# Kernel optimization log

Measured on AMD Instinct MI355X. Metric: run time of the kernel, lower is better.

Reference implementation:

```python
import jax, jax.numpy as jnp
import numpy as np

B, N, P, K, D = 8, 2048, 64, 32, 384
DEPTH, DI, DS, DCONV, DTR, NC = 12, 768, 16, 4, 24, 40
BN_EPS = 1e-5


def _spread_bits(v):
    v = v & 1023
    v = (v | (v << 16)) & 50331903
    v = (v | (v << 8)) & 50393103
    v = (v | (v << 4)) & 51130563
    v = (v | (v << 2)) & 153391689
    return v


def _zkey(x, y, z):
    return _spread_bits(x) | (_spread_bits(y) << 1) | (_spread_bits(z) << 2)


def _sfc_order(xyz, trans):
    lo = xyz.min(0, keepdims=True)
    hi = xyz.max(0, keepdims=True)
    q = jnp.clip(((xyz - lo) / (hi - lo + 1e-6) * 1023.0).astype(jnp.int32), 0, 1023)
    if trans:
        keys = _zkey(q[:, 2], q[:, 1], q[:, 0])
    else:
        keys = _zkey(q[:, 0], q[:, 1], q[:, 2])
    return jnp.argsort(keys)


def _ln(x, g, b):
    m = x.mean(-1, keepdims=True)
    v = jnp.var(x, axis=-1, keepdims=True)
    return (x - m) / jnp.sqrt(v + 1e-5) * g + b


def _bn_eval(x, g, b):
    # BatchNorm in eval mode, running_mean=0 / running_var=1
    return x * (g / np.float32(np.sqrt(1.0 + BN_EPS))) + b


def _patch_embed_one(xyz, w1, b1, g1, be1, w2, b2, g2, be2, w3, b3, g3, be3):
    # xyz: (N,3)
    cidx = (jnp.arange(P) * (N / P)).astype(jnp.int32)
    centers = xyz[cidx]                                      # (P,3)
    d2 = ((centers[:, None, :] - xyz[None, :, :]) ** 2).sum(-1)  # (P,N)
    _, knn = jax.lax.top_k(-d2, K)                           # (P,K) smallest dists
    nx = xyz[knn] - centers[:, None, :]                      # (P,K,3)
    h = jax.nn.gelu(_bn_eval(nx @ w1.T + b1, g1, be1), approximate=False)   # (P,K,64)
    h = jax.nn.gelu(_bn_eval(h @ w2.T + b2, g2, be2), approximate=False)    # (P,K,128)
    h = _bn_eval(h @ w3.T + b3, g3, be3)                     # (P,K,384)
    return h.max(1), centers


def _mamba(x, in_w, conv_w, conv_b, xp_w, dt_w, dt_b, Alog, Dp, out_w):
    # x: (B,L,D)
    Bsz, L, _ = x.shape
    xz = x @ in_w.T                                          # (B,L,2*DI)
    xc, z = xz[..., :DI], xz[..., DI:]
    xpad = jnp.pad(xc, ((0, 0), (DCONV - 1, 0), (0, 0)))
    xc = sum(xpad[:, j:j + L, :] * conv_w[:, j] for j in range(DCONV)) + conv_b
    xc = jax.nn.silu(xc)
    x_dbl = xc @ xp_w.T                                      # (B,L,DTR+2*DS)
    dt = x_dbl[..., :DTR]
    Bm = x_dbl[..., DTR:DTR + DS]
    Cm = x_dbl[..., DTR + DS:]
    delta = jax.nn.softplus(dt @ dt_w.T + dt_b)              # (B,L,DI)
    A = -jnp.exp(Alog)                                       # (DI,DS)

    def step(h, inp):
        d_t, B_t, C_t, u_t = inp                             # (B,DI),(B,DS),(B,DS),(B,DI)
        h = h * jnp.exp(d_t[..., None] * A) + (d_t * u_t)[..., None] * B_t[:, None, :]
        return h, jnp.einsum('bds,bs->bd', h, C_t)

    h0 = jnp.zeros((Bsz, DI, DS), x.dtype)
    inps = (delta.transpose(1, 0, 2), Bm.transpose(1, 0, 2),
            Cm.transpose(1, 0, 2), xc.transpose(1, 0, 2))
    _, ys = jax.lax.scan(step, h0, inps)                     # (L,B,DI)
    y = ys.transpose(1, 0, 2) + Dp * xc
    y = y * jax.nn.silu(z)
    return y @ out_w.T


def setup_inputs() -> dict:
    key = jax.random.key(0)
    ks = iter(jax.random.split(key, 64))
    nrm = lambda *s: jax.random.normal(next(ks), s, jnp.float32) * 0.02
    inp = {
        'data': jax.random.normal(next(ks), (B, N, 3), jnp.float32),
        'pe_w1': nrm(64, 3), 'pe_b1': jnp.zeros(64), 'pe_g1': jnp.ones(64), 'pe_be1': jnp.zeros(64),
        'pe_w2': nrm(128, 64), 'pe_b2': jnp.zeros(128), 'pe_g2': jnp.ones(128), 'pe_be2': jnp.zeros(128),
        'pe_w3': nrm(D, 128), 'pe_b3': jnp.zeros(D), 'pe_g3': jnp.ones(D), 'pe_be3': jnp.zeros(D),
        'oi_h_scale': jnp.ones(D), 'oi_h_shift': jnp.zeros(D),
        'oi_th_scale': jnp.ones(D), 'oi_th_shift': jnp.zeros(D),
        'pos_embed': nrm(1, P, D),
        'blk_ln_g': jnp.ones((DEPTH, D)), 'blk_ln_b': jnp.zeros((DEPTH, D)),
        'blk_in_w': nrm(DEPTH, 2 * DI, D),
        'blk_conv_w': nrm(DEPTH, DI, DCONV), 'blk_conv_b': jnp.zeros((DEPTH, DI)),
        'blk_xp_w': nrm(DEPTH, DTR + 2 * DS, DI),
        'blk_dt_w': nrm(DEPTH, DI, DTR), 'blk_dt_b': jnp.full((DEPTH, DI), -4.0),
        'blk_Alog': jnp.tile(jnp.log(jnp.arange(1, DS + 1, dtype=jnp.float32)), (DEPTH, DI, 1)),
        'blk_D': jnp.ones((DEPTH, DI)),
        'blk_out_w': nrm(DEPTH, D, DI),
        'norm_g': jnp.ones(D), 'norm_b': jnp.zeros(D),
        'mlp_w1': nrm(256, D), 'mlp_b1': jnp.zeros(256),
        'mlp_w2': nrm(64, 256), 'mlp_b2': jnp.zeros(64),
        'mlp_w3': nrm(NC, 64), 'mlp_b3': jnp.zeros(NC),
    }
    return inp


def reference(data, pe_w1, pe_b1, pe_g1, pe_be1, pe_w2, pe_b2, pe_g2, pe_be2,
              pe_w3, pe_b3, pe_g3, pe_be3, oi_h_scale, oi_h_shift, oi_th_scale,
              oi_th_shift, pos_embed, blk_ln_g, blk_ln_b, blk_in_w, blk_conv_w,
              blk_conv_b, blk_xp_w, blk_dt_w, blk_dt_b, blk_Alog, blk_D,
              blk_out_w, norm_g, norm_b, mlp_w1, mlp_b1, mlp_w2, mlp_b2,
              mlp_w3, mlp_b3):
    xyz = data[:, :, :3]
    tokens, centers = jax.vmap(
        _patch_embed_one, in_axes=(0,) + (None,) * 12)(
        xyz, pe_w1, pe_b1, pe_g1, pe_be1, pe_w2, pe_b2, pe_g2, pe_be2,
        pe_w3, pe_b3, pe_g3, pe_be3)                         # (B,P,D),(B,P,3)
    order_h = jax.vmap(lambda c: _sfc_order(c, False))(centers)
    order_th = jax.vmap(lambda c: _sfc_order(c, True))(centers)
    th = jnp.take_along_axis(tokens, order_h[:, :, None], axis=1) * oi_h_scale + oi_h_shift
    tth = jnp.take_along_axis(tokens, order_th[:, :, None], axis=1) * oi_th_scale + oi_th_shift
    t = jnp.concatenate([th + pos_embed, tth + pos_embed], axis=1)  # (B,2P,D)
    for i in range(DEPTH):
        t = t + _mamba(_ln(t, blk_ln_g[i], blk_ln_b[i]),
                       blk_in_w[i], blk_conv_w[i], blk_conv_b[i], blk_xp_w[i],
                       blk_dt_w[i], blk_dt_b[i], blk_Alog[i], blk_D[i], blk_out_w[i])
    t = _ln(t, norm_g, norm_b)
    x = t.mean(1)
    x = jax.nn.relu(x @ mlp_w1.T + mlp_b1)
    x = jax.nn.relu(x @ mlp_w2.T + mlp_b2)
    return x @ mlp_w3.T + mlp_b3
```

## Files before the change

### kernel.cpp

```cpp
#include <hip/hip_runtime.h>
#include <math.h>

#define BB 8
#define NN 2048
#define PP 64
#define KK 32
#define DD 384
#define DEPTH 12
#define DI 768
#define DS 16
#define DCONV 4
#define DTR 24
#define NC 40
#define LL 128
#define XROW (DTR + 2 * DS)
#define NR (BB * LL)

using bf16x8 = __attribute__((ext_vector_type(8))) short;
using floatx4 = __attribute__((ext_vector_type(4))) float;

__device__ __forceinline__ float gelu_exact(float x) {
    return 0.5f * x * (1.0f + erff(x * 0.70710678118654752440f));
}
__device__ __forceinline__ float siluf(float x) {
    return x / (1.0f + expf(-x));
}
__device__ __forceinline__ unsigned short f2bf(float f) {
    unsigned u = __float_as_uint(f);
    u += 0x7fffu + ((u >> 16) & 1u);
    return (unsigned short)(u >> 16);
}
__device__ __forceinline__ float bf2f(short s) {
    return __uint_as_float(((unsigned)(unsigned short)s) << 16);
}
__device__ __forceinline__ unsigned spread_bits(unsigned v) {
    v &= 1023u;
    v = (v | (v << 16)) & 50331903u;
    v = (v | (v << 8)) & 50393103u;
    v = (v | (v << 4)) & 51130563u;
    v = (v | (v << 2)) & 153391689u;
    return v;
}

__global__ void k_cvt(const float* __restrict__ in_w, const float* __restrict__ out_w,
                      const float* __restrict__ pe_w3, const float* __restrict__ xp,
                      unsigned short* __restrict__ inwbf, unsigned short* __restrict__ owbf,
                      unsigned short* __restrict__ w3bf, unsigned short* __restrict__ xpbf)
{
    int idx = (blockIdx.x * 256 + threadIdx.x) * 4;
    const int n1 = DEPTH * 2 * DI * DD;
    const int n2 = DEPTH * DD * DI;
    const int n3 = DD * 128;
    const int n4 = DEPTH * 64 * DI;
    if (idx < n1) {
        float4 v = *(const float4*)(in_w + idx);
        ushort4 o; o.x = f2bf(v.x); o.y = f2bf(v.y); o.z = f2bf(v.z); o.w = f2bf(v.w);
        *(ushort4*)(inwbf + idx) = o;
        return;
    }
    idx -= n1;
    if (idx < n2) {
        float4 v = *(const float4*)(out_w + idx);
        ushort4 o; o.x = f2bf(v.x); o.y = f2bf(v.y); o.z = f2bf(v.z); o.w = f2bf(v.w);
        *(ushort4*)(owbf + idx) = o;
        return;
    }
    idx -= n2;
    if (idx < n3) {
        float4 v = *(const float4*)(pe_w3 + idx);
        ushort4 o; o.x = f2bf(v.x); o.y = f2bf(v.y); o.z = f2bf(v.z); o.w = f2bf(v.w);
        *(ushort4*)(w3bf + idx) = o;
        return;
    }
    idx -= n3;
    if (idx < n4) {
        int i = idx / (64 * DI);
        int rem = idx - i * 64 * DI;
        int n = rem / DI, k = rem % DI;
        ushort4 o;
        if (n < XROW) {
            float4 v = *(const float4*)(xp + (size_t)i * XROW * DI + (size_t)n * DI + k);
            o.x = f2bf(v.x); o.y = f2bf(v.y); o.z = f2bf(v.z); o.w = f2bf(v.w);
        } else {
            o.x = o.y = o.z = o.w = 0;
        }
        *(ushort4*)(xpbf + (size_t)i * 64 * DI + (size_t)n * DI + k) = o;
    }
}

__global__ __launch_bounds__(256) void k_patch(
    const float* __restrict__ data,
    const float* __restrict__ w1, const float* __restrict__ b1,
    const float* __restrict__ g1, const float* __restrict__ be1,
    const float* __restrict__ w2, const float* __restrict__ b2,
    const float* __restrict__ g2, const float* __restrict__ be2,
    const unsigned short* __restrict__ w3bf, const float* __restrict__ b3,
    const float* __restrict__ g3, const float* __restrict__ be3,
    float* __restrict__ tokens, float* __restrict__ centers)
{
    const int bp = blockIdx.x;
    const int b = bp >> 6, p = bp & 63;
    const int tid = threadIdx.x;
    const float* X = data + (size_t)b * NN * 3;
    const float inv_den = 0.99999500003749968752f;

    __shared__ unsigned long long wred[4];
    __shared__ int klist[KK];
    __shared__ float nxs[KK * 3];
    __shared__ float h1s[KK * 64];
    __shared__ short h2b[KK * 136];

    const float cx = X[p * 32 * 3 + 0];
    const float cy = X[p * 32 * 3 + 1];
    const float cz = X[p * 32 * 3 + 2];
    if (tid == 0) {
        centers[(b * PP + p) * 3 + 0] = cx;
        centers[(b * PP + p) * 3 + 1] = cy;
        centers[(b * PP + p) * 3 + 2] = cz;
    }

    {
        const int lane = tid & 63, wid = tid >> 6;
        unsigned long long pk[8];
#pragma unroll
        for (int q = 0; q < 8; q++) {
            int i = tid + 256 * q;
            float dx = cx - X[i * 3 + 0];
            float dy = cy - X[i * 3 + 1];
            float dz = cz - X[i * 3 + 2];
            float d2 = dx * dx + dy * dy + dz * dz;
            pk[q] = ((unsigned long long)__float_as_uint(d2) << 32) | (unsigned)i;
        }
        for (int k = 0; k < KK; k++) {
            unsigned long long m = pk[0];
#pragma unroll
            for (int q = 1; q < 8; q++) m = pk[q] < m ? pk[q] : m;
#pragma unroll
            for (int off = 32; off; off >>= 1) {
                unsigned long long o = __shfl_xor(m, off);
                m = o < m ? o : m;
            }
            if (lane == 0) wred[wid] = m;
            __syncthreads();
            unsigned long long g = wred[0];
#pragma unroll
            for (int w = 1; w < 4; w++) g = wred[w] < g ? wred[w] : g;
#pragma unroll
            for (int q = 0; q < 8; q++)
                if (pk[q] == g) pk[q] = ~0ull;
            if (tid == 0) klist[k] = (int)(g & 0xffffffffu);
            __syncthreads();
        }
    }

    if (tid < KK) {
        int q = klist[tid];
        nxs[tid * 3 + 0] = X[q * 3 + 0] - cx;
        nxs[tid * 3 + 1] = X[q * 3 + 1] - cy;
        nxs[tid * 3 + 2] = X[q * 3 + 2] - cz;
    }
    __syncthreads();

    for (int e = tid; e < KK * 64; e += 256) {
        int j = e >> 6, c = e & 63;
        float v = nxs[j * 3 + 0] * w1[c * 3 + 0] + nxs[j * 3 + 1] * w1[c * 3 + 1] +
                  nxs[j * 3 + 2] * w1[c * 3 + 2] + b1[c];
        v = v * (g1[c] * inv_den) + be1[c];
        h1s[j * 64 + c] = gelu_exact(v);
    }
    __syncthreads();

    for (int e = tid; e < KK * 128; e += 256) {
        int j = e >> 7, c = e & 127;
        const float4* wr = (const float4*)(w2 + (size_t)c * 64);
        const float4* hr = (const float4*)(h1s + j * 64);
        float acc = 0.f;
#pragma unroll
        for (int q = 0; q < 16; q++) {
            float4 wv = wr[q], hv = hr[q];
            acc += hv.x * wv.x + hv.y * wv.y + hv.z * wv.z + hv.w * wv.w;
        }
        float v = (acc + b2[c]) * (g2[c] * inv_den) + be2[c];
        h2b[j * 136 + c] = (short)f2bf(gelu_exact(v));
    }
    __syncthreads();

    const int wave = tid >> 6, lane = tid & 63;
    const int quad = lane >> 4, r = lane & 15;
    floatx4 acc3[2][6] = {};
#pragma unroll
    for (int ks = 0; ks < 4; ks++) {
        const int k0 = ks * 32;
        bf16x8 af[2];
        af[0] = *(const bf16x8*)(h2b + (size_t)r * 136 + quad * 8 + k0);
        af[1] = *(const bf16x8*)(h2b + (size_t)(16 + r) * 136 + quad * 8 + k0);
        bf16x8 bfv[6];
#pragma unroll
        for (int nj = 0; nj < 6; nj++) {
            int n = wave * 96 + nj * 16 + r;
            bfv[nj] = *(const bf16x8*)(w3bf + (size_t)n * 128 + quad * 8 + k0);
        }
#pragma unroll
        for (int mi = 0; mi < 2; mi++)
#pragma unroll
            for (int nj = 0; nj < 6; nj++)
                acc3[mi][nj] = __builtin_amdgcn_mfma_f32_16x16x32_bf16(af[mi], bfv[nj], acc3[mi][nj], 0, 0, 0);
    }
#pragma unroll
    for (int nj = 0; nj < 6; nj++) {
        int col = wave * 96 + nj * 16 + r;
        float sc = g3[col] * inv_den;
        float offc = b3[col] * sc + be3[col];
        float m = -3.4e38f;
#pragma unroll
        for (int mi = 0; mi < 2; mi++)
#pragma unroll
            for (int r2 = 0; r2 < 4; r2++)
                m = fmaxf(m, acc3[mi][nj][r2] * sc + offc);
        m = fmaxf(m, __shfl_xor(m, 16));
        m = fmaxf(m, __shfl_xor(m, 32));
        if (quad == 0) tokens[(size_t)bp * DD + col] = m;
    }
}

__global__ __launch_bounds__(256) void k_sfc_build(
    const float* __restrict__ centers, const float* __restrict__ tokens,
    const float* __restrict__ hs, const float* __restrict__ hb,
    const float* __restrict__ ts2, const float* __restrict__ tb2,
    const float* __restrict__ pos, float* __restrict__ tout)
{
    const int b = blockIdx.y, part = blockIdx.x;
    const int tid = threadIdx.x;

    __shared__ float csh[PP][3];
    __shared__ float slo[3], shi[3];
    __shared__ unsigned khs[PP], kts[PP];
    __shared__ int oh[PP], ot[PP];

    if (tid < PP) {
        csh[tid][0] = centers[(b * PP + tid) * 3 + 0];
        csh[tid][1] = centers[(b * PP + tid) * 3 + 1];
        csh[tid][2] = centers[(b * PP + tid) * 3 + 2];
    }
    __syncthreads();
    if (tid == 0) {
        for (int k = 0; k < 3; k++) {
            float lo = csh[0][k], hi = csh[0][k];
            for (int j = 1; j < PP; j++) { lo = fminf(lo, csh[j][k]); hi = fmaxf(hi, csh[j][k]); }
            slo[k] = lo; shi[k] = hi;
        }
    }
    __syncthreads();
    if (tid < PP) {
        int q[3];
        for (int k = 0; k < 3; k++) {
            float t = (csh[tid][k] - slo[k]) / (shi[k] - slo[k] + 1e-6f) * 1023.0f;
            int qi = (int)t;
            qi = qi < 0 ? 0 : (qi > 1023 ? 1023 : qi);
            q[k] = qi;
        }
        khs[tid] = spread_bits((unsigned)q[0]) | (spread_bits((unsigned)q[1]) << 1) |
                   (spread_bits((unsigned)q[2]) << 2);
        kts[tid] = spread_bits((unsigned)q[2]) | (spread_bits((unsigned)q[1]) << 1) |
                   (spread_bits((unsigned)q[0]) << 2);
    }
    __syncthreads();
    if (tid < PP) {
        unsigned kh = khs[tid], kt = kts[tid];
        int rh = 0, rt = 0;
        for (int j = 0; j < PP; j++) {
            unsigned a = khs[j];
            rh += (a < kh) || (a == kh && j < tid);
            unsigned c = kts[j];
            rt += (c < kt) || (c == kt && j < tid);
        }
        oh[rh] = tid;
        ot[rt] = tid;
    }
    __syncthreads();

    const int base = part * (LL * DD / 24);
    for (int e = tid; e < LL * DD / 24; e += 256) {
        int idx = base + e;
        int d = idx % DD;
        int l = idx / DD;
        float v;
        if (l < PP) {
            int src = oh[l];
            v = tokens[((size_t)b * PP + src) * DD + d] * hs[d] + hb[d] + pos[l * DD + d];
        } else {
            int l2 = l - PP;
            int src = ot[l2];
            v = tokens[((size_t)b * PP + src) * DD + d] * ts2[d] + tb2[d] + pos[l2 * DD + d];
        }
        tout[(size_t)b * LL * DD + idx] = v;
    }
}

__global__ __launch_bounds__(256) void k_stats(const float* __restrict__ t,
                                               const float* __restrict__ g,
                                               const float* __restrict__ gb,
                                               unsigned short* __restrict__ tbf,
                                               float* __restrict__ xdbl)
{
    const int tid = threadIdx.x;
    {
        int gi = blockIdx.x * 256 + tid;
        if (gi < NR * XROW) xdbl[gi] = 0.f;
    }
    const int wid = tid >> 6, lane = tid & 63;
    const int row = blockIdx.x * 4 + wid;
    const size_t base = (size_t)row * DD;
    float v[6];
    float s = 0.f, q = 0.f;
#pragma unroll
    for (int j = 0; j < 6; j++) {
        v[j] = t[base + lane + 64 * j];
        s += v[j]; q += v[j] * v[j];
    }
#pragma unroll
    for (int off = 32; off; off >>= 1) { s += __shfl_xor(s, off); q += __shfl_xor(q, off); }
    float mean = s * (1.0f / DD);
    float var = q * (1.0f / DD) - mean * mean;
    float inv = 1.0f / sqrtf(var + 1e-5f);
#pragma unroll
    for (int j = 0; j < 6; j++) {
        int i = lane + 64 * j;
        tbf[base + i] = f2bf((v[j] - mean) * inv * g[i] + gb[i]);
    }
}

__global__ __launch_bounds__(256) void k_mfma_xz(
    const unsigned short* __restrict__ tbf,
    const unsigned short* __restrict__ inwbf,
    const float* __restrict__ cw, const float* __restrict__ cb,
    const unsigned short* __restrict__ xpbf,
    unsigned short* __restrict__ xcbf, unsigned short* __restrict__ zsbf,
    float* __restrict__ xdbl)
{
    __shared__ short ct[128][72];
    const int tid = threadIdx.x;
    const int wave = tid >> 6, lane = tid & 63;
    const int quad = lane >> 4, r = lane & 15;
    const int wm = wave >> 1, wn = wave & 1;
    const int b = blockIdx.y;
    const int n0 = blockIdx.x * 64;
    const int m0 = b * 128 + wm * 64;

    floatx4 acc[4][2] = {};
    const unsigned short* Ab = tbf + (size_t)(m0 + r) * DD + quad * 8;
    const unsigned short* Bb = inwbf + (size_t)(n0 + wn * 32 + r) * DD + quad * 8;
    for (int k0 = 0; k0 < DD; k0 += 32) {
        bf16x8 af[4], bfv[2];
#pragma unroll
        for (int i = 0; i < 4; i++)
            af[i] = *(const bf16x8*)(Ab + (size_t)(i * 16) * DD + k0);
#pragma unroll
        for (int j = 0; j < 2; j++)
            bfv[j] = *(const bf16x8*)(Bb + (size_t)(j * 16) * DD + k0);
#pragma unroll
        for (int i = 0; i < 4; i++)
#pragma unroll
            for (int j = 0; j < 2; j++)
                acc[i][j] = __builtin_amdgcn_mfma_f32_16x16x32_bf16(af[i], bfv[j], acc[i][j], 0, 0, 0);
    }

#pragma unroll
    for (int i = 0; i < 4; i++)
#pragma unroll
        for (int r2 = 0; r2 < 4; r2++) {
            short* cp = &ct[wm * 64 + i * 16 + quad * 4 + r2][wn * 32 + r];
#pragma unroll
            for (int j = 0; j < 2; j++)
                cp[j * 16] = (short)f2bf(acc[i][j][r2]);
        }
    __syncthreads();

    const int l0 = (tid >> 3) * 4;
    const int c0 = (tid & 7) * 8;
    if (n0 < DI) {
        float cwv[8][4], cbv[8];
#pragma unroll
        for (int q = 0; q < 8; q++) {
            *(float4*)cwv[q] = *(const float4*)(cw + (size_t)(n0 + c0 + q) * 4);
            cbv[q] = cb[n0 + c0 + q];
        }
        unsigned short ov[4][8];
#pragma unroll
        for (int dl = 0; dl < 4; dl++) {
            const int l = l0 + dl;
            float u[8];
#pragma unroll
            for (int q = 0; q < 8; q++) u[q] = cbv[q];
#pragma unroll
            for (int j = 0; j < DCONV; j++) {
                int lt = l - (DCONV - 1) + j;
                if (lt >= 0) {
                    bf16x8 x = *(const bf16x8*)&ct[lt][c0];
#pragma unroll
                    for (int q = 0; q < 8; q++) u[q] += bf2f(x[q]) * cwv[q][j];
                }
            }
#pragma unroll
            for (int q = 0; q < 8; q++) ov[dl][q] = f2bf(siluf(u[q]));
        }
        __syncthreads();
#pragma unroll
        for (int dl = 0; dl < 4; dl++) {
            const int l = l0 + dl;
            *(bf16x8*)&ct[l][c0] = *(bf16x8*)ov[dl];
            *(bf16x8*)(xcbf + (size_t)(b * LL + l) * DI + n0 + c0) = *(bf16x8*)ov[dl];
        }
        __syncthreads();

        floatx4 acc2[2][4] = {};
#pragma unroll
        for (int k0 = 0; k0 < 64; k0 += 32) {
            bf16x8 af2[2], bfv2[4];
#pragma unroll
            for (int i = 0; i < 2; i++)
                af2[i] = *(const bf16x8*)&ct[wave * 32 + i * 16 + r][k0 + quad * 8];
#pragma unroll
            for (int nj = 0; nj < 4; nj++)
                bfv2[nj] = *(const bf16x8*)(xpbf + (size_t)(nj * 16 + r) * DI + n0 + k0 + quad * 8);
#pragma unroll
            for (int i = 0; i < 2; i++)
#pragma unroll
                for (int nj = 0; nj < 4; nj++)
                    acc2[i][nj] = __builtin_amdgcn_mfma_f32_16x16x32_bf16(af2[i], bfv2[nj], acc2[i][nj], 0, 0, 0);
        }
#pragma unroll
        for (int i = 0; i < 2; i++)
#pragma unroll
            for (int nj = 0; nj < 4; nj++) {
                int col = nj * 16 + r;
                if (col < XROW) {
#pragma unroll
                    for (int r2 = 0; r2 < 4; r2++) {
                        int row = b * LL + wave * 32 + i * 16 + quad * 4 + r2;
                        unsafeAtomicAdd(&xdbl[(size_t)row * XROW + col], acc2[i][nj][r2]);
                    }
                }
            }
    } else {
        const int nz = n0 - DI;
#pragma unroll
        for (int dl = 0; dl < 4; dl++) {
            const int l = l0 + dl;
            bf16x8 x = *(const bf16x8*)&ct[l][c0];
            unsigned short o[8];
#pragma unroll
            for (int q = 0; q < 8; q++) o[q] = f2bf(siluf(bf2f(x[q])));
            *(bf16x8*)(zsbf + (size_t)(b * LL + l) * DI + nz + c0) = *(bf16x8*)o;
        }
    }
}

__global__ __launch_bounds__(128) void k_scan(
    const float* __restrict__ xdbl,
    const unsigned short* __restrict__ xcbf, const unsigned short* __restrict__ zsbf,
    const float* __restrict__ dtw, const float* __restrict__ dtb,
    const float* __restrict__ Alog, const float* __restrict__ Dp,
    unsigned short* __restrict__ ybf)
{
    const int tid = threadIdx.x;
    const int b = blockIdx.x / DI;
    const int d = blockIdx.x % DI;

    __shared__ float sdel[LL];
    __shared__ float sdus[LL];
    __shared__ float sus[LL];
    __shared__ float szs[LL];
    __shared__ float negA[DS];
    __shared__ float ApL[DS][9];
    __shared__ float HlL[DS][9];
    __shared__ float hst[DS][9];

    {
        const int t = tid;
        const size_t row = (size_t)b * LL + t;
        const float* xd = xdbl + row * XROW;
        const float* w = dtw + d * DTR;
        float acc = dtb[d];
#pragma unroll
        for (int k = 0; k < DTR; k += 4) {
            float4 xv = *(const float4*)(xd + k);
            float4 wv = *(const float4*)(w + k);
            acc += xv.x * wv.x + xv.y * wv.y + xv.z * wv.z + xv.w * wv.w;
        }
        float delta = fmaxf(acc, 0.f) + log1pf(__expf(-fabsf(acc)));
        float u = bf2f((short)xcbf[row * DI + d]);
        sdel[t] = delta;
        sdus[t] = delta * u;
        sus[t] = u;
        szs[t] = bf2f((short)zsbf[row * DI + d]);
    }
    if (tid < DS) negA[tid] = -__expf(Alog[d * DS + tid]);
    __syncthreads();

    const int s = tid & 15;
    const int c = tid >> 4;
    const float* xB = xdbl + ((size_t)b * LL + c * 16) * XROW + DTR + s;

    float a_r[16], duB_r[16], C_r[16];
    {
        float h = 0.f, Ap = 1.f;
        const float na = negA[s];
#pragma unroll
        for (int q = 0; q < 16; q++) {
            int t = c * 16 + q;
            float a = __expf(sdel[t] * na);
            float Bv = xB[(size_t)q * XROW];
            float Cv = xB[(size_t)q * XROW + DS];
            a_r[q] = a;
            duB_r[q] = sdus[t] * Bv;
            C_r[q] = Cv;
            h = h * a + duB_r[q];
            Ap *= a;
        }
        ApL[s][c] = Ap;
        HlL[s][c] = h;
    }
    __syncthreads();
    if (tid < DS) {
        float hs = 0.f;
#pragma unroll
        for (int cc = 0; cc < 8; cc++) {
            hst[tid][cc] = hs;
            hs = ApL[tid][cc] * hs + HlL[tid][cc];
        }
    }
    __syncthreads();

    {
        const float Dd = Dp[d];
        float h = hst[s][c];
        unsigned short* yc = ybf + ((size_t)b * LL + c * 16) * DI + d;
#pragma unroll
        for (int q = 0; q < 16; q++) {
            h = h * a_r[q] + duB_r[q];
            float p = h * C_r[q];
            p += __shfl_xor(p, 1, 16);
            p += __shfl_xor(p, 2, 16);
            p += __shfl_xor(p, 4, 16);
            p += __shfl_xor(p, 8, 16);
            if (s == 0) {
                int t = c * 16 + q;
                yc[(size_t)q * DI] = f2bf((p + Dd * sus[t]) * szs[t]);
            }
        }
    }
}

__global__ __launch_bounds__(256) void k_mfma_op(
    const unsigned short* __restrict__ ybf,
    const unsigned short* __restrict__ owbf,
    float* __restrict__ t)
{
    const int tid = threadIdx.x;
    const int wave = tid >> 6, lane = tid & 63;
    const int quad = lane >> 4, r = lane & 15;
    const int wr2 = wave >> 1, wc = wave & 1;
    const int n0 = blockIdx.x * 64 + wc * 32;
    const int m0 = blockIdx.y * 32 + wr2 * 16;

    floatx4 acc[2] = {};
    const unsigned short* Ab = ybf + (size_t)(m0 + r) * DI + quad * 8;
    const unsigned short* Bb = owbf + (size_t)(n0 + r) * DI + quad * 8;
    for (int k0 = 0; k0 < DI; k0 += 32) {
        bf16x8 af = *(const bf16x8*)(Ab + k0);
        bf16x8 b0 = *(const bf16x8*)(Bb + k0);
        bf16x8 b1 = *(const bf16x8*)(Bb + (size_t)16 * DI + k0);
        acc[0] = __builtin_amdgcn_mfma_f32_16x16x32_bf16(af, b0, acc[0], 0, 0, 0);
        acc[1] = __builtin_amdgcn_mfma_f32_16x16x32_bf16(af, b1, acc[1], 0, 0, 0);
    }

#pragma unroll
    for (int j = 0; j < 2; j++) {
        int col = n0 + j * 16 + r;
#pragma unroll
        for (int r2 = 0; r2 < 4; r2++) {
            int row = m0 + quad * 4 + r2;
            float* tp = t + (size_t)row * DD + col;
            *tp += acc[j][r2];
        }
    }
}

__global__ __launch_bounds__(256) void k_lnpool(const float* __restrict__ t,
                                                const float* __restrict__ ng,
                                                const float* __restrict__ nb,
                                                float* __restrict__ pparts)
{
    const int b = blockIdx.y, chunk = blockIdx.x;
    const int tid = threadIdx.x;
    const int wave = tid >> 6, lane = tid & 63;
    __shared__ float pw[4][DD];

    for (int c = lane; c < DD; c += 64) pw[wave][c] = 0.f;
    __syncthreads();

    for (int rr = 0; rr < 4; rr++) {
        const int row = b * LL + chunk * 16 + wave * 4 + rr;
        const float* xr = t + (size_t)row * DD;
        float v[6];
        float s = 0.f, q = 0.f;
#pragma unroll
        for (int j = 0; j < 6; j++) { v[j] = xr[lane + 64 * j]; s += v[j]; q += v[j] * v[j]; }
#pragma unroll
        for (int off = 32; off; off >>= 1) { s += __shfl_xor(s, off); q += __shfl_xor(q, off); }
        float mean = s * (1.0f / DD);
        float var = q * (1.0f / DD) - mean * mean;
        float inv = 1.0f / sqrtf(var + 1e-5f);
#pragma unroll
        for (int j = 0; j < 6; j++) {
            int c = lane + 64 * j;
            pw[wave][c] += (v[j] - mean) * inv * ng[c] + nb[c];
        }
    }
    __syncthreads();
    float* out = pparts + ((size_t)b * 8 + chunk) * DD;
    for (int c = tid; c < DD; c += 256)
        out[c] = pw[0][c] + pw[1][c] + pw[2][c] + pw[3][c];
}

__global__ __launch_bounds__(256) void k_mlp(const float* __restrict__ pparts,
    const float* __restrict__ w1, const float* __restrict__ b1,
    const float* __restrict__ w2, const float* __restrict__ b2,
    const float* __restrict__ w3, const float* __restrict__ b3,
    float* __restrict__ out)
{
    const int b = blockIdx.x, tid = threadIdx.x;
    __shared__ float pl[DD];
    __shared__ float h1[256];
    __shared__ float h2[64];
    for (int c = tid; c < DD; c += 256) {
        const float* pp = pparts + (size_t)b * 8 * DD + c;
        float s = 0.f;
#pragma unroll
        for (int z = 0; z < 8; z++) s += pp[z * DD];
        pl[c] = s * (1.0f / LL);
    }
    __syncthreads();

    {
        float acc = b1[tid];
        const float* wr = w1 + (size_t)tid * DD;
        for (int k = 0; k < DD; k++) acc += pl[k] * wr[k];
        h1[tid] = fmaxf(acc, 0.f);
    }
    __syncthreads();
    if (tid < 64) {
        float acc = b2[tid];
        const float* wr = w2 + (size_t)tid * 256;
        for (int k = 0; k < 256; k++) acc += h1[k] * wr[k];
        h2[tid] = fmaxf(acc, 0.f);
    }
    __syncthreads();
    if (tid < NC) {
        float acc = b3[tid];
        const float* wr = w3 + (size_t)tid * 64;
        for (int k = 0; k < 64; k++) acc += h2[k] * wr[k];
        out[b * NC + tid] = acc;
    }
}

extern "C" void kernel_launch(void* const* d_in, const int* in_sizes, int n_in,
                              void* d_out, int out_size, void* d_ws, size_t ws_size,
                              hipStream_t stream)
{
    const float* data      = (const float*)d_in[0];
    const float* pe_w1     = (const float*)d_in[1];
    const float* pe_b1     = (const float*)d_in[2];
    const float* pe_g1     = (const float*)d_in[3];
    const float* pe_be1    = (const float*)d_in[4];
    const float* pe_w2     = (const float*)d_in[5];
    const float* pe_b2     = (const float*)d_in[6];
    const float* pe_g2     = (const float*)d_in[7];
    const float* pe_be2    = (const float*)d_in[8];
    const float* pe_w3     = (const float*)d_in[9];
    const float* pe_b3     = (const float*)d_in[10];
    const float* pe_g3     = (const float*)d_in[11];
    const float* pe_be3    = (const float*)d_in[12];
    const float* oi_h_scale  = (const float*)d_in[13];
    const float* oi_h_shift  = (const float*)d_in[14];
    const float* oi_th_scale = (const float*)d_in[15];
    const float* oi_th_shift = (const float*)d_in[16];
    const float* pos_embed = (const float*)d_in[17];
    const float* blk_ln_g  = (const float*)d_in[18];
    const float* blk_ln_b  = (const float*)d_in[19];
    const float* blk_in_w  = (const float*)d_in[20];
    const float* blk_conv_w = (const float*)d_in[21];
    const float* blk_conv_b = (const float*)d_in[22];
    const float* blk_xp_w  = (const float*)d_in[23];
    const float* blk_dt_w  = (const float*)d_in[24];
    const float* blk_dt_b  = (const float*)d_in[25];
    const float* blk_Alog  = (const float*)d_in[26];
    const float* blk_D     = (const float*)d_in[27];
    const float* blk_out_w = (const float*)d_in[28];
    const float* norm_g    = (const float*)d_in[29];
    const float* norm_b    = (const float*)d_in[30];
    const float* mlp_w1    = (const float*)d_in[31];
    const float* mlp_b1    = (const float*)d_in[32];
    const float* mlp_w2    = (const float*)d_in[33];
    const float* mlp_b2    = (const float*)d_in[34];
    const float* mlp_w3    = (const float*)d_in[35];
    const float* mlp_b3    = (const float*)d_in[36];

    float* ws = (float*)d_ws;
    size_t off = 0;
    auto alloc = [&](size_t n) { float* p = ws + off; off += (n + 63) & ~(size_t)63; return p; };
    float* tokens  = alloc((size_t)BB * PP * DD);
    float* centers = alloc((size_t)BB * PP * 3);
    float* t    = alloc((size_t)NR * DD);
    float* xdbl = alloc((size_t)NR * XROW);
    float* pparts  = alloc((size_t)BB * 8 * DD);
    unsigned short* tbf   = (unsigned short*)alloc((size_t)NR * DD / 2);
    unsigned short* xcbf  = (unsigned short*)alloc((size_t)NR * DI / 2);
    unsigned short* zsbf  = (unsigned short*)alloc((size_t)NR * DI / 2);
    unsigned short* ybf   = (unsigned short*)alloc((size_t)NR * DI / 2);
    unsigned short* inwbf = (unsigned short*)alloc((size_t)DEPTH * 2 * DI * DD / 2);
    unsigned short* owbf  = (unsigned short*)alloc((size_t)DEPTH * DD * DI / 2);
    unsigned short* xpbf  = (unsigned short*)alloc((size_t)DEPTH * 64 * DI / 2);
    unsigned short* w3bf  = (unsigned short*)alloc((size_t)DD * 128 / 2);

    {
        const int total = DEPTH * 2 * DI * DD + DEPTH * DD * DI + DD * 128 + DEPTH * 64 * DI;
        k_cvt<<<(total / 4 + 255) / 256, 256, 0, stream>>>(
            blk_in_w, blk_out_w, pe_w3, blk_xp_w, inwbf, owbf, w3bf, xpbf);
    }

    k_patch<<<BB * PP, 256, 0, stream>>>(data,
        pe_w1, pe_b1, pe_g1, pe_be1, pe_w2, pe_b2, pe_g2, pe_be2,
        w3bf, pe_b3, pe_g3, pe_be3, tokens, centers);
    k_sfc_build<<<dim3(24, BB), 256, 0, stream>>>(centers, tokens,
        oi_h_scale, oi_h_shift, oi_th_scale, oi_th_shift, pos_embed, t);

    for (int i = 0; i < DEPTH; i++) {
        const float* ln_g = blk_ln_g + i * DD;
        const float* ln_b = blk_ln_b + i * DD;
        const float* cw   = blk_conv_w + (size_t)i * DI * DCONV;
        const float* cb   = blk_conv_b + (size_t)i * DI;
        const float* dtw  = blk_dt_w + (size_t)i * DI * DTR;
        const float* dtb  = blk_dt_b + (size_t)i * DI;
        const float* Al   = blk_Alog + (size_t)i * DI * DS;
        const float* Dpp  = blk_D + (size_t)i * DI;
        const unsigned short* inw = inwbf + (size_t)i * 2 * DI * DD;
        const unsigned short* ow  = owbf + (size_t)i * DD * DI;
        const unsigned short* xpb = xpbf + (size_t)i * 64 * DI;

        k_stats<<<NR / 4, 256, 0, stream>>>(t, ln_g, ln_b, tbf, xdbl);
        k_mfma_xz<<<dim3(24, BB), 256, 0, stream>>>(
            tbf, inw, cw, cb, xpb, xcbf, zsbf, xdbl);
        k_scan<<<BB * DI, 128, 0, stream>>>(xdbl, xcbf, zsbf, dtw, dtb, Al, Dpp, ybf);
        k_mfma_op<<<dim3(DD / 64, NR / 32), 256, 0, stream>>>(ybf, ow, t);
    }

    k_lnpool<<<dim3(8, BB), 256, 0, stream>>>(t, norm_g, norm_b, pparts);
    k_mlp<<<BB, 256, 0, stream>>>(pparts, mlp_w1, mlp_b1, mlp_w2, mlp_b2, mlp_w3, mlp_b3,
                                  (float*)d_out);
}
```

Before: 960.6 us.

## Replace iterative kNN argmin with radix select and split-K out-projection

The kNN selection in the patch kernel swaps 32 rounds of block-wide argmin reductions for a 4-pass byte-wise radix select over distance keys. Keys below the threshold are collected with atomics, and ties are broken by index on a single thread. Separately, the out-projection GEMM is split over K into two halves that accumulate into the residual with float atomics, which doubles the block count. The atomic accumulation makes float summation order nondeterministic, and neighbour order in klist changes, though the max-pool downstream does not depend on it.

Measured after the change: 937.9 us. -2.4%, faster.

```diff
diff --git a/kernel.cpp b/kernel.cpp
--- a/kernel.cpp
+++ b/kernel.cpp
@@ -104,8 +104,10 @@
     const float* X = data + (size_t)b * NN * 3;
     const float inv_den = 0.99999500003749968752f;
 
-    __shared__ unsigned long long wred[4];
+    __shared__ int hist[256];
     __shared__ int klist[KK];
+    __shared__ int eqlist[256];
+    __shared__ int s_kth, s_byte, s_cnt, s_eqcnt;
     __shared__ float nxs[KK * 3];
     __shared__ float h1s[KK * 64];
     __shared__ short h2b[KK * 136];
@@ -117,11 +119,12 @@
         centers[(b * PP + p) * 3 + 0] = cx;
         centers[(b * PP + p) * 3 + 1] = cy;
         centers[(b * PP + p) * 3 + 2] = cz;
+        s_kth = KK; s_cnt = 0; s_eqcnt = 0;
     }
 
     {
         const int lane = tid & 63, wid = tid >> 6;
-        unsigned long long pk[8];
+        unsigned key[8];
 #pragma unroll
         for (int q = 0; q < 8; q++) {
             int i = tid + 256 * q;
@@ -129,28 +132,71 @@
             float dy = cy - X[i * 3 + 1];
             float dz = cz - X[i * 3 + 2];
             float d2 = dx * dx + dy * dy + dz * dz;
-            pk[q] = ((unsigned long long)__float_as_uint(d2) << 32) | (unsigned)i;
-        }
-        for (int k = 0; k < KK; k++) {
-            unsigned long long m = pk[0];
-#pragma unroll
-            for (int q = 1; q < 8; q++) m = pk[q] < m ? pk[q] : m;
-#pragma unroll
-            for (int off = 32; off; off >>= 1) {
-                unsigned long long o = __shfl_xor(m, off);
-                m = o < m ? o : m;
+            key[q] = __float_as_uint(d2);
+        }
+        unsigned prefix = 0;
+        for (int rnd = 3; rnd >= 0; rnd--) {
+            const int sh = rnd * 8;
+            const unsigned pmask = (rnd == 3) ? 0u : (0xFFFFFFFFu << (8 * (rnd + 1)));
+            hist[tid] = 0;
+            __syncthreads();
+#pragma unroll
+            for (int q = 0; q < 8; q++)
+                if ((key[q] & pmask) == prefix)
+                    atomicAdd(&hist[(key[q] >> sh) & 255], 1);
+            __syncthreads();
+            if (wid == 0) {
+                int c[4], tot = 0;
+#pragma unroll
+                for (int j = 0; j < 4; j++) { c[j] = hist[lane * 4 + j]; tot += c[j]; }
+                int inc = tot;
+#pragma unroll
+                for (int off = 1; off < 64; off <<= 1) {
+                    int u = __shfl_up(inc, off);
+                    if (lane >= off) inc += u;
+                }
+                int exc = inc - tot;
+                int kth = s_kth;
+                bool has = (exc < kth) && (exc + tot >= kth);
+                unsigned long long bal = __ballot(has);
+                int src = __ffsll(bal) - 1;
+                if (lane == src) {
+                    int rem = kth - exc;
+                    int j = 0, cum = 0;
+                    while (cum + c[j] < rem) { cum += c[j]; j++; }
+                    s_byte = lane * 4 + j;
+                    s_kth = rem - cum;
+                }
             }
-            if (lane == 0) wred[wid] = m;
             __syncthreads();
-            unsigned long long g = wred[0];
-#pragma unroll
-            for (int w = 1; w < 4; w++) g = wred[w] < g ? wred[w] : g;
-#pragma unroll
-            for (int q = 0; q < 8; q++)
-                if (pk[q] == g) pk[q] = ~0ull;
-            if (tid == 0) klist[k] = (int)(g & 0xffffffffu);
-            __syncthreads();
-        }
+            prefix |= ((unsigned)s_byte) << sh;
+        }
+        const unsigned kstar = prefix;
+        const int need = s_kth;
+#pragma unroll
+        for (int q = 0; q < 8; q++) {
+            int i = tid + 256 * q;
+            if (key[q] < kstar) {
+                int pos = atomicAdd(&s_cnt, 1);
+                klist[pos] = i;
+            } else if (key[q] == kstar) {
+                int pos = atomicAdd(&s_eqcnt, 1);
+                if (pos < 256) eqlist[pos] = i;
+            }
+        }
+        __syncthreads();
+        if (tid == 0) {
+            int base = s_cnt;
+            int ne = s_eqcnt < 256 ? s_eqcnt : 256;
+            for (int k = 0; k < need; k++) {
+                int best = 0x7fffffff, bi = 0;
+                for (int j = 0; j < ne; j++)
+                    if (eqlist[j] < best) { best = eqlist[j]; bi = j; }
+                klist[base + k] = best;
+                eqlist[bi] = 0x7fffffff;
+            }
+        }
+        __syncthreads();
     }
 
     if (tid < KK) {
@@ -563,11 +609,12 @@
     const int wr2 = wave >> 1, wc = wave & 1;
     const int n0 = blockIdx.x * 64 + wc * 32;
     const int m0 = blockIdx.y * 32 + wr2 * 16;
+    const int kb = blockIdx.z * (DI / 2);
 
     floatx4 acc[2] = {};
-    const unsigned short* Ab = ybf + (size_t)(m0 + r) * DI + quad * 8;
-    const unsigned short* Bb = owbf + (size_t)(n0 + r) * DI + quad * 8;
-    for (int k0 = 0; k0 < DI; k0 += 32) {
+    const unsigned short* Ab = ybf + (size_t)(m0 + r) * DI + kb + quad * 8;
+    const unsigned short* Bb = owbf + (size_t)(n0 + r) * DI + kb + quad * 8;
+    for (int k0 = 0; k0 < DI / 2; k0 += 32) {
         bf16x8 af = *(const bf16x8*)(Ab + k0);
         bf16x8 b0 = *(const bf16x8*)(Bb + k0);
         bf16x8 b1 = *(const bf16x8*)(Bb + (size_t)16 * DI + k0);
@@ -581,8 +628,7 @@
 #pragma unroll
         for (int r2 = 0; r2 < 4; r2++) {
             int row = m0 + quad * 4 + r2;
-            float* tp = t + (size_t)row * DD + col;
-            *tp += acc[j][r2];
+            unsafeAtomicAdd(t + (size_t)row * DD + col, acc[j][r2]);
         }
     }
 }
@@ -753,7 +799,7 @@
         k_mfma_xz<<<dim3(24, BB), 256, 0, stream>>>(
             tbf, inw, cw, cb, xpb, xcbf, zsbf, xdbl);
         k_scan<<<BB * DI, 128, 0, stream>>>(xdbl, xcbf, zsbf, dtw, dtb, Al, Dpp, ybf);
-        k_mfma_op<<<dim3(DD / 64, NR / 32), 256, 0, stream>>>(ybf, ow, t);
+        k_mfma_op<<<dim3(DD / 64, NR / 32, 2), 256, 0, stream>>>(ybf, ow, t);
     }
 
     k_lnpool<<<dim3(8, BB), 256, 0, stream>>>(t, norm_g, norm_b, pparts);
```
